# Performance work log

Hardware: AMD Instinct MI355X
Metric: run time of the kernel (lower is better)

The kernel has to match this reference:

```python
import jax, jax.numpy as jnp
import numpy as np

B, H, S, D = 2, 12, 4096, 768
BS = 64              # block size
HD = D // H          # head dim = 64
NB = S // BS         # 64 blocks
MC = 3               # max graph connections per block
PEN = -10000.0
RSQRT_D = 1.0 / np.sqrt(HD).astype(np.float32)


def setup_inputs() -> dict:
    key = jax.random.key(0)
    ks = jax.random.split(key, 6)
    hidden_states = jax.random.normal(ks[0], (B, S, D), jnp.float32)
    Wq = jax.random.normal(ks[1], (D, D), jnp.float32) * 0.02
    Wk = jax.random.normal(ks[2], (D, D), jnp.float32) * 0.02
    Wv = jax.random.normal(ks[3], (D, D), jnp.float32) * 0.02
    Wo = jax.random.normal(ks[4], (D, D), jnp.float32) * 0.02
    graph_attn = jax.random.randint(ks[5], (B, H, NB, MC), 0, NB, jnp.int32)
    return dict(
        hidden_states=hidden_states, Wq=Wq, Wk=Wk, Wv=Wv, Wo=Wo,
        band_mask=jnp.ones((B, 1, NB - 4, BS, 3 * BS), jnp.float32),
        from_mask=jnp.ones((B, 1, S, 1), jnp.float32),
        to_mask=jnp.ones((B, 1, 1, S), jnp.float32),
        from_blocked_mask=jnp.ones((B, NB, BS), jnp.float32),
        to_blocked_mask=jnp.ones((B, NB, BS), jnp.float32),
        graph_attn=graph_attn,
    )


def reference(hidden_states, Wq, Wk, Wv, Wo, band_mask, from_mask, to_mask,
              from_blocked_mask, to_blocked_mask, graph_attn):
    def proj(W):  # [B,S,D] -> [B,H,S,HD]
        return (hidden_states @ W.T).reshape(B, S, H, HD).transpose(0, 2, 1, 3)

    q, k, v = proj(Wq), proj(Wk), proj(Wv)
    bq = q.reshape(B, H, NB, BS, HD)
    bk = k.reshape(B, H, NB, BS, HD)
    bv = v.reshape(B, H, NB, BS, HD)

    # gather graph-selected key/value blocks: [B,H,NB,MC*BS,HD]
    gather = jax.vmap(jax.vmap(lambda blocks, idx: blocks[idx]))
    gk = gather(bk, graph_attn).reshape(B, H, NB, MC * BS, HD)
    gv = gather(bv, graph_attn).reshape(B, H, NB, MC * BS, HD)

    # graph mask from blocked masks: [B,H,NB,BS,MC*BS]
    gm = jax.vmap(lambda tm, ga: tm[ga])(to_blocked_mask, graph_attn)  # [B,H,NB,MC,BS]
    gm = gm.reshape(B, H, NB, MC * BS)
    graph_mask = jnp.einsum('blq,bhlk->bhlqk', from_blocked_mask, gm)

    # ---- first block: global attention over all keys ----
    fp = jnp.einsum('bhqd,bhkd->bhqk', bq[:, :, 0], k) * RSQRT_D + (1.0 - to_mask) * PEN
    first_ctx = jnp.einsum('bhqk,bhkd->bhqd', jax.nn.softmax(fp, -1), v)[:, :, None]

    # ---- second block: blocks 0,1,2,last + graph-gathered ----
    sk = jnp.concatenate([bk[:, :, 0], bk[:, :, 1], bk[:, :, 2], bk[:, :, -1], gk[:, :, 1]], axis=2)
    sv = jnp.concatenate([bv[:, :, 0], bv[:, :, 1], bv[:, :, 2], bv[:, :, -1], gv[:, :, 1]], axis=2)
    sp = jnp.einsum('bhqd,bhkd->bhqk', bq[:, :, 1], sk) * RSQRT_D
    seq_pad = jnp.concatenate([to_mask[:, :, :, :3 * BS], to_mask[:, :, :, -BS:],
                               jnp.ones((B, 1, 1, MC * BS), to_mask.dtype)], axis=3)
    rand_pad = jnp.concatenate([jnp.ones((B, H, BS, 4 * BS), graph_mask.dtype),
                                graph_mask[:, :, 1]], axis=3)
    sp = sp + (1.0 - jnp.minimum(seq_pad, rand_pad)) * PEN
    second_ctx = jnp.einsum('bhqk,bhkd->bhqd', jax.nn.softmax(sp, -1), sv)[:, :, None]

    # ---- middle blocks: sliding window (3 blocks) + first + last + graph ----
    ek = jnp.concatenate([bk[:, :, 1:-3], bk[:, :, 2:-2], bk[:, :, 3:-1]], axis=3)  # [B,H,NB-4,3BS,HD]
    ev = jnp.concatenate([bv[:, :, 1:-3], bv[:, :, 2:-2], bv[:, :, 3:-1]], axis=3)
    qm = bq[:, :, 2:-2]
    inner = jnp.einsum('bhlqd,bhlkd->bhlqk', qm, ek) * RSQRT_D + (1.0 - band_mask) * PEN
    randp = jnp.einsum('bhlqd,bhlkd->bhlqk', qm, gk[:, :, 2:-2]) * RSQRT_D + (1.0 - graph_mask[:, :, 2:-2]) * PEN
    firstp = jnp.einsum('bhlqd,bhkd->bhlqk', qm, bk[:, :, 0]) * RSQRT_D + (1.0 - to_mask[:, :, :, None, :BS]) * PEN
    lastp = jnp.einsum('bhlqd,bhkd->bhlqk', qm, bk[:, :, -1]) * RSQRT_D + (1.0 - to_mask[:, :, :, None, -BS:]) * PEN
    band = jnp.concatenate([firstp, inner, randp, lastp], axis=-1)
    attn = jax.nn.softmax(band, -1)
    mid_ctx = (jnp.einsum('bhlqk,bhlkd->bhlqd', attn[..., BS:4 * BS], ev)
               + jnp.einsum('bhlqk,bhlkd->bhlqd', attn[..., 4 * BS:4 * BS + MC * BS], gv[:, :, 2:-2])
               + jnp.einsum('bhlqk,bhkd->bhlqd', attn[..., :BS], bv[:, :, 0])
               + jnp.einsum('bhlqk,bhkd->bhlqd', attn[..., -BS:], bv[:, :, -1]))

    # ---- second-to-last block ----
    slk = jnp.concatenate([bk[:, :, 0], bk[:, :, -3], bk[:, :, -2], bk[:, :, -1], gk[:, :, -2]], axis=2)
    slv = jnp.concatenate([bv[:, :, 0], bv[:, :, -3], bv[:, :, -2], bv[:, :, -1], gv[:, :, -2]], axis=2)
    slp = jnp.einsum('bhqd,bhkd->bhqk', bq[:, :, -2], slk) * RSQRT_D
    sl_seq = jnp.concatenate([to_mask[:, :, :, :BS], to_mask[:, :, :, -3 * BS:],
                              jnp.ones((B, 1, 1, MC * BS), to_mask.dtype)], axis=3)
    sl_rand = jnp.concatenate([jnp.ones((B, H, BS, 4 * BS), graph_mask.dtype),
                               graph_mask[:, :, -2]], axis=3)
    slp = slp + (1.0 - jnp.minimum(sl_seq, sl_rand)) * PEN
    sl_ctx = jnp.einsum('bhqk,bhkd->bhqd', jax.nn.softmax(slp, -1), slv)[:, :, None]

    # ---- last block: global attention over all keys ----
    lp = jnp.einsum('bhqd,bhkd->bhqk', bq[:, :, -1], k) * RSQRT_D + (1.0 - to_mask) * PEN
    last_ctx = jnp.einsum('bhqk,bhkd->bhqd', jax.nn.softmax(lp, -1), v)[:, :, None]

    ctx = jnp.concatenate([first_ctx, second_ctx, mid_ctx, sl_ctx, last_ctx], axis=2)
    ctx = ctx.reshape(B, H, S, HD) * from_mask            # [B,H,S,HD]
    ctx = ctx.transpose(0, 2, 1, 3).reshape(B, S, D)      # [B,S,D]
    return ctx @ Wo.T                                     # output projection (no bias)
```

## Files before the change

kernel.cpp:

```cpp
#include <hip/hip_runtime.h>
#include <hip/hip_bf16.h>

#define BB 2
#define HH 12
#define SS 4096
#define DD 768
#define HD 64
#define NBK 64
#define MC 3

typedef __attribute__((ext_vector_type(8))) short short8_t;
typedef __attribute__((ext_vector_type(4))) float float4_t;

__device__ __forceinline__ unsigned short f2bf(float f) {
  union { float f; unsigned u; } c;
  c.f = f;
  unsigned u = c.u + 0x7FFFu + ((c.u >> 16) & 1u);
  return (unsigned short)(u >> 16);
}

__device__ __forceinline__ void gload16(const unsigned short* gp,
                                        unsigned short* lp) {
  __builtin_amdgcn_global_load_lds(
      (const __attribute__((address_space(1))) unsigned int*)gp,
      (__attribute__((address_space(3))) unsigned int*)lp, 16, 0, 0);
}

#define LDK 72

__global__ __launch_bounds__(256) void cvt_all(
    const float* __restrict__ hs, const float* __restrict__ Wq,
    const float* __restrict__ Wk, const float* __restrict__ Wv,
    const float* __restrict__ Wo, unsigned short* __restrict__ hsb,
    unsigned short* __restrict__ wqkvb, unsigned short* __restrict__ wob) {
  long i4 = (long)blockIdx.x * 256 + threadIdx.x;
  const float* src;
  unsigned short* dst;
  if (i4 < 1572864) {
    src = hs + i4 * 4;
    dst = hsb + i4 * 4;
  } else {
    long r = i4 - 1572864;
    int w = (int)(r / 147456);
    long e = r % 147456;
    src = (w == 0 ? Wq : w == 1 ? Wk : w == 2 ? Wv : Wo) + e * 4;
    dst = (w < 3) ? (wqkvb + (long)w * 589824 + e * 4) : (wob + e * 4);
  }
  float4_t v = *(const float4_t*)src;
  uint2 p;
  p.x = (unsigned)f2bf(v[0]) | ((unsigned)f2bf(v[1]) << 16);
  p.y = (unsigned)f2bf(v[2]) | ((unsigned)f2bf(v[3]) << 16);
  *(uint2*)dst = p;
}

#define STAGE_T(buf_, A_, B_, m0_, n0_, kt_)                                  \
  {                                                                           \
    int rr_ = lane >> 3;                                                      \
    int cg_ = (lane & 7) ^ rr_;                                               \
    _Pragma("unroll") for (int u = 0; u < 4; u++) {                           \
      int g_ = w * 4 + u;                                                     \
      gload16(A_ + (size_t)(m0_ + g_ * 8 + rr_) * DD + kt_ + cg_ * 8,         \
              &As[buf_][g_ * 512]);                                           \
    }                                                                         \
    _Pragma("unroll") for (int u = 0; u < 2; u++) {                           \
      int g_ = w * 2 + u;                                                     \
      gload16(B_ + (size_t)(n0_ + g_ * 8 + rr_) * DD + kt_ + cg_ * 8,         \
              &Bs[buf_][g_ * 512]);                                           \
    }                                                                         \
  }

#define LOAD_FRAGS2(buf_, kk_)                                                \
  int cb = qd + ((kk_) >> 3);                                                 \
  short8_t af[2], bfr[4];                                                     \
  _Pragma("unroll") for (int i = 0; i < 2; i++) {                             \
    int r_ = wm + i * 16 + fr;                                                \
    af[i] = *(const short8_t*)&As[buf_][r_ * 64 + (cb ^ (fr & 7)) * 8];       \
  }                                                                           \
  _Pragma("unroll") for (int j = 0; j < 4; j++) {                             \
    int r_ = j * 16 + fr;                                                     \
    bfr[j] = *(const short8_t*)&Bs[buf_][r_ * 64 + (cb ^ (fr & 7)) * 8];      \
  }

__global__ __launch_bounds__(256) void gemm_qkv_b(
    const unsigned short* __restrict__ A, const unsigned short* __restrict__ W,
    unsigned short* __restrict__ qb, unsigned short* __restrict__ kb,
    unsigned short* __restrict__ vtb) {
  __shared__ unsigned short As[2][128 * 64];
  __shared__ unsigned short Bs[2][64 * 64];
  int tid = threadIdx.x;
  int m0 = blockIdx.x * 128;
  int n0 = blockIdx.y * 64;
  int lane = tid & 63;
  int w = tid >> 6;
  int wm = w * 32;
  int fr = lane & 15;
  int qd = lane >> 4;
  int ysel = n0 / 768;

  float4_t acc[8];
#pragma unroll
  for (int i = 0; i < 8; i++)
#pragma unroll
    for (int r = 0; r < 4; r++) acc[i][r] = 0.f;

  STAGE_T(0, A, W, m0, n0, 0)
  int p = 0;

  if (ysel < 2) {
    for (int kt = 0; kt < DD; kt += 64) {
      __syncthreads();
      if (kt + 64 < DD) STAGE_T(p ^ 1, A, W, m0, n0, kt + 64)
#pragma unroll
      for (int kk = 0; kk < 64; kk += 32) {
        LOAD_FRAGS2(p, kk)
#pragma unroll
        for (int i = 0; i < 2; i++)
#pragma unroll
          for (int j = 0; j < 4; j++)
            acc[j * 2 + i] = __builtin_amdgcn_mfma_f32_16x16x32_bf16(
                bfr[j], af[i], acc[j * 2 + i], 0, 0, 0);
      }
      p ^= 1;
    }
    int cn = lane & 15;
    int quad = lane >> 4;
    float scale = (ysel == 0) ? 0.125f : 1.0f;
    unsigned short* dst = (ysel == 0) ? qb : kb;
    int nb0 = n0 - ysel * 768;
#pragma unroll
    for (int j = 0; j < 4; j++)
#pragma unroll
      for (int i = 0; i < 2; i++) {
        int m = m0 + wm + i * 16 + cn;
        int nn = nb0 + j * 16 + quad * 4;
        int b = m >> 12, s = m & 4095;
        int h = nn >> 6, d0 = nn & 63;
        uint2 pk;
        pk.x = (unsigned)f2bf(acc[j * 2 + i][0] * scale) |
               ((unsigned)f2bf(acc[j * 2 + i][1] * scale) << 16);
        pk.y = (unsigned)f2bf(acc[j * 2 + i][2] * scale) |
               ((unsigned)f2bf(acc[j * 2 + i][3] * scale) << 16);
        *(uint2*)&dst[(((size_t)b * HH + h) * SS + s) * HD + d0] = pk;
      }
  } else {
    for (int kt = 0; kt < DD; kt += 64) {
      __syncthreads();
      if (kt + 64 < DD) STAGE_T(p ^ 1, A, W, m0, n0, kt + 64)
#pragma unroll
      for (int kk = 0; kk < 64; kk += 32) {
        LOAD_FRAGS2(p, kk)
#pragma unroll
        for (int i = 0; i < 2; i++)
#pragma unroll
          for (int j = 0; j < 4; j++)
            acc[i * 4 + j] = __builtin_amdgcn_mfma_f32_16x16x32_bf16(
                af[i], bfr[j], acc[i * 4 + j], 0, 0, 0);
      }
      p ^= 1;
    }
    int cn = lane & 15;
    int quad = lane >> 4;
    int nb0 = n0 - 1536;
#pragma unroll
    for (int i = 0; i < 2; i++)
#pragma unroll
      for (int j = 0; j < 4; j++) {
        int m = m0 + wm + i * 16 + quad * 4;
        int nn = nb0 + j * 16 + cn;
        int b = m >> 12, s0 = m & 4095;
        int h = nn >> 6, d = nn & 63;
        uint2 pk;
        pk.x = (unsigned)f2bf(acc[i * 4 + j][0]) |
               ((unsigned)f2bf(acc[i * 4 + j][1]) << 16);
        pk.y = (unsigned)f2bf(acc[i * 4 + j][2]) |
               ((unsigned)f2bf(acc[i * 4 + j][3]) << 16);
        *(uint2*)&vtb[(((size_t)b * HH + h) * HD + d) * SS + s0] = pk;
      }
  }
}

__global__ __launch_bounds__(256) void gemm_out_b(
    const unsigned short* __restrict__ A, const unsigned short* __restrict__ W,
    float* __restrict__ dst) {
  __shared__ unsigned short As[2][128 * 64];
  __shared__ unsigned short Bs[2][64 * 64];
  int tid = threadIdx.x;
  int m0 = blockIdx.x * 128;
  int n0 = blockIdx.y * 64;
  int lane = tid & 63;
  int w = tid >> 6;
  int wm = w * 32;
  int fr = lane & 15;
  int qd = lane >> 4;

  float4_t acc[8];
#pragma unroll
  for (int i = 0; i < 8; i++)
#pragma unroll
    for (int r = 0; r < 4; r++) acc[i][r] = 0.f;

  STAGE_T(0, A, W, m0, n0, 0)
  int p = 0;
  for (int kt = 0; kt < DD; kt += 64) {
    __syncthreads();
    if (kt + 64 < DD) STAGE_T(p ^ 1, A, W, m0, n0, kt + 64)
#pragma unroll
    for (int kk = 0; kk < 64; kk += 32) {
      LOAD_FRAGS2(p, kk)
#pragma unroll
      for (int i = 0; i < 2; i++)
#pragma unroll
        for (int j = 0; j < 4; j++)
          acc[i * 4 + j] = __builtin_amdgcn_mfma_f32_16x16x32_bf16(
              af[i], bfr[j], acc[i * 4 + j], 0, 0, 0);
    }
    p ^= 1;
  }

  int cn = lane & 15;
  int rb = (lane >> 4) * 4;
#pragma unroll
  for (int i = 0; i < 2; i++)
#pragma unroll
    for (int j = 0; j < 4; j++)
#pragma unroll
      for (int r = 0; r < 4; r++) {
        int m = m0 + wm + i * 16 + rb + r;
        int n = n0 + j * 16 + cn;
        dst[(size_t)m * DD + n] = acc[i * 4 + j][r];
      }
}

__global__ __launch_bounds__(256) void attn2(
    const unsigned short* __restrict__ q, const unsigned short* __restrict__ k,
    const unsigned short* __restrict__ vt, const int* __restrict__ graph,
    unsigned short* __restrict__ ctxb, float* __restrict__ part) {
  __shared__ unsigned short Ks[2][64 * LDK];
  __shared__ unsigned short Vs[2][64 * LDK];
  __shared__ unsigned short Ps[4][16 * LDK];

  int tid = threadIdx.x;
  int id = blockIdx.x;
  int b, h, l, nkb, heavy, chunk = 0, hid = 0;
  int list[8];
  if (id < 384) {
    heavy = 1;
    hid = id >> 3;
    chunk = id & 7;
    b = hid / 24;
    int r = hid % 24;
    h = r >> 1;
    l = (r & 1) ? (NBK - 1) : 0;
    nkb = 8;
#pragma unroll
    for (int i = 0; i < 8; i++) list[i] = chunk * 8 + i;
  } else {
    heavy = 0;
    int j = id - 384;
    b = j / 744;
    int r = j % 744;
    h = r / 62;
    l = 1 + r % 62;
    const int* g = graph + (((size_t)b * HH + h) * NBK + l) * MC;
    int n = 0;
    if (l == 1) {
      list[0] = 0; list[1] = 1; list[2] = 2; list[3] = NBK - 1; n = 4;
    } else if (l == NBK - 2) {
      list[0] = 0; list[1] = NBK - 3; list[2] = NBK - 2; list[3] = NBK - 1; n = 4;
    } else {
      list[0] = 0; list[1] = l - 1; list[2] = l; list[3] = l + 1;
      list[4] = NBK - 1; n = 5;
    }
    for (int m = 0; m < MC; m++) list[n++] = g[m];
    nkb = n;
  }
  size_t base = ((size_t)b * HH + h) * SS * HD;

  int lane = tid & 63;
  int w = tid >> 6;
  int lr = lane & 15;
  int quad = lane >> 4;

  short8_t qa[2];
  {
    const unsigned short* qp =
        q + base + (size_t)(l * 64 + w * 16 + lr) * HD + quad * 8;
    qa[0] = *(const short8_t*)qp;
    qa[1] = *(const short8_t*)(qp + 32);
  }

  float4_t Ot[4];
  float ls[4];
#pragma unroll
  for (int t = 0; t < 4; t++)
#pragma unroll
    for (int r = 0; r < 4; r++) Ot[t][r] = 0.f;
#pragma unroll
  for (int r = 0; r < 4; r++) ls[r] = 0.f;

  int srow = tid >> 3;
  int scol = (tid & 7) * 8;

  uint4 kr0, kr1, vr0, vr1;
  {
    int kb = list[0];
    const unsigned short* kp = k + base + (size_t)(kb * 64 + srow) * HD + scol;
    const unsigned short* vp = vt + base + (size_t)srow * SS + kb * 64 + scol;
    kr0 = *(const uint4*)kp;
    kr1 = *(const uint4*)(kp + 32 * HD);
    vr0 = *(const uint4*)vp;
    vr1 = *(const uint4*)(vp + 32 * SS);
  }
  *(uint4*)&Ks[0][srow * LDK + scol] = kr0;
  *(uint4*)&Ks[0][(srow + 32) * LDK + scol] = kr1;
  *(uint4*)&Vs[0][srow * LDK + scol] = vr0;
  *(uint4*)&Vs[0][(srow + 32) * LDK + scol] = vr1;
  int p = 0;

  for (int t = 0; t < nkb; t++) {
    __syncthreads();

    if (t + 1 < nkb) {
      int kb = list[t + 1];
      const unsigned short* kp = k + base + (size_t)(kb * 64 + srow) * HD + scol;
      const unsigned short* vp = vt + base + (size_t)srow * SS + kb * 64 + scol;
      kr0 = *(const uint4*)kp;
      kr1 = *(const uint4*)(kp + 32 * HD);
      vr0 = *(const uint4*)vp;
      vr1 = *(const uint4*)(vp + 32 * SS);
    }

    float4_t st[4];
#pragma unroll
    for (int tt = 0; tt < 4; tt++) {
#pragma unroll
      for (int r = 0; r < 4; r++) st[tt][r] = 0.f;
      short8_t kb0 = *(const short8_t*)&Ks[p][(tt * 16 + lr) * LDK + quad * 8];
      short8_t kb1 =
          *(const short8_t*)&Ks[p][(tt * 16 + lr) * LDK + quad * 8 + 32];
      st[tt] = __builtin_amdgcn_mfma_f32_16x16x32_bf16(qa[0], kb0, st[tt], 0, 0, 0);
      st[tt] = __builtin_amdgcn_mfma_f32_16x16x32_bf16(qa[1], kb1, st[tt], 0, 0, 0);
    }

#pragma unroll
    for (int tt = 0; tt < 4; tt++)
#pragma unroll
      for (int r = 0; r < 4; r++) {
        float pv = __expf(st[tt][r]);
        st[tt][r] = pv;
        ls[r] += pv;
        Ps[w][(quad * 4 + r) * LDK + tt * 16 + lr] = f2bf(pv);
      }

#pragma unroll
    for (int s = 0; s < 2; s++) {
      short8_t pa = *(const short8_t*)&Ps[w][lr * LDK + s * 32 + quad * 8];
#pragma unroll
      for (int tt = 0; tt < 4; tt++) {
        short8_t vb =
            *(const short8_t*)&Vs[p][(tt * 16 + lr) * LDK + s * 32 + quad * 8];
        Ot[tt] = __builtin_amdgcn_mfma_f32_16x16x32_bf16(pa, vb, Ot[tt], 0, 0, 0);
      }
    }

    if (t + 1 < nkb) {
      *(uint4*)&Ks[p ^ 1][srow * LDK + scol] = kr0;
      *(uint4*)&Ks[p ^ 1][(srow + 32) * LDK + scol] = kr1;
      *(uint4*)&Vs[p ^ 1][srow * LDK + scol] = vr0;
      *(uint4*)&Vs[p ^ 1][(srow + 32) * LDK + scol] = vr1;
    }
    p ^= 1;
  }

#pragma unroll
  for (int r = 0; r < 4; r++)
#pragma unroll
    for (int off = 1; off < 16; off <<= 1) ls[r] += __shfl_xor(ls[r], off);

  if (!heavy) {
#pragma unroll
    for (int r = 0; r < 4; r++) {
      float inv = 1.f / ls[r];
      size_t row = (size_t)b * SS + (size_t)l * 64 + w * 16 + quad * 4 + r;
#pragma unroll
      for (int tt = 0; tt < 4; tt++)
        ctxb[row * DD + h * HD + tt * 16 + lr] = f2bf(Ot[tt][r] * inv);
    }
  } else {
    float* pb = part + ((size_t)hid * 8 + chunk) * 4160;
#pragma unroll
    for (int r = 0; r < 4; r++) {
      int rowi = w * 16 + quad * 4 + r;
#pragma unroll
      for (int tt = 0; tt < 4; tt++)
        pb[rowi * 64 + tt * 16 + lr] = Ot[tt][r];
      if (lr == 0) pb[4096 + rowi] = ls[r];
    }
  }
}

__global__ __launch_bounds__(256) void reduce_heavy(
    const float* __restrict__ part, unsigned short* __restrict__ ctxb) {
  __shared__ float lrow[64];
  int hid = blockIdx.x;
  int tid = threadIdx.x;
  int b = hid / 24;
  int r = hid % 24;
  int h = r >> 1;
  int l = (r & 1) ? (NBK - 1) : 0;
  const float* pb = part + (size_t)hid * 8 * 4160;
  if (tid < 64) {
    float s = 0.f;
#pragma unroll
    for (int c = 0; c < 8; c++) s += pb[c * 4160 + 4096 + tid];
    lrow[tid] = s;
  }
  __syncthreads();
#pragma unroll
  for (int e = tid; e < 4096; e += 256) {
    float o = 0.f;
#pragma unroll
    for (int c = 0; c < 8; c++) o += pb[c * 4160 + e];
    int rowi = e >> 6, col = e & 63;
    size_t row = (size_t)b * SS + (size_t)l * 64 + rowi;
    ctxb[row * DD + h * HD + col] = f2bf(o / lrow[rowi]);
  }
}

extern "C" void kernel_launch(void* const* d_in, const int* in_sizes, int n_in,
                              void* d_out, int out_size, void* d_ws,
                              size_t ws_size, hipStream_t stream) {
  const float* hs = (const float*)d_in[0];
  const float* Wq = (const float*)d_in[1];
  const float* Wk = (const float*)d_in[2];
  const float* Wv = (const float*)d_in[3];
  const float* Wo = (const float*)d_in[4];
  const int* graph = (const int*)d_in[10];

  const size_t NHS = (size_t)BB * SS * DD;
  unsigned short* hsb = (unsigned short*)d_ws;
  unsigned short* wqkvb = hsb + NHS;
  unsigned short* wob = wqkvb + 3 * 768 * 768;
  unsigned short* qb = wob + 768 * 768;
  unsigned short* kb = qb + NHS;
  unsigned short* vtb = kb + NHS;
  unsigned short* ctxb = vtb + NHS;
  float* part = (float*)(ctxb + NHS);

  cvt_all<<<8448, 256, 0, stream>>>(hs, Wq, Wk, Wv, Wo, hsb, wqkvb, wob);
  gemm_qkv_b<<<dim3(64, 36, 1), 256, 0, stream>>>(hsb, wqkvb, qb, kb, vtb);
  attn2<<<1872, 256, 0, stream>>>(qb, kb, vtb, graph, ctxb, part);
  reduce_heavy<<<48, 256, 0, stream>>>(part, ctxb);
  gemm_out_b<<<dim3(64, 12, 1), 256, 0, stream>>>(ctxb, wob, (float*)d_out);
}
```

Before: 209.5 us.

## Fuse fp32-to-bf16 conversion into GEMMs and fold heavy-row reduction into attention

Drops the separate conversion kernel. The QKV and output GEMMs now read fp32 inputs and weights directly, convert them to bf16 in registers with v_cvt_pk_bf16_f32, and store them into swizzled LDS. The separate reduce_heavy launch is replaced by an atomic-counter last-block reduction inside the attention kernel, and the QKV GEMM zeroes the counters. This saves a full read/write pass over the bf16 copies and two launches, at the cost of twice the global load bytes per GEMM tile, register-staged loads instead of direct-to-LDS loads, and the weights being reconverted by every tile.

```diff
diff --git a/kernel.cpp b/kernel.cpp
--- a/kernel.cpp
+++ b/kernel.cpp
@@ -8,6 +8,7 @@
 #define HD 64
 #define NBK 64
 #define MC 3
+#define LDK 72
 
 typedef __attribute__((ext_vector_type(8))) short short8_t;
 typedef __attribute__((ext_vector_type(4))) float float4_t;
@@ -19,6 +20,12 @@
   return (unsigned short)(u >> 16);
 }
 
+__device__ __forceinline__ unsigned cvtpk(float lo, float hi) {
+  unsigned r;
+  asm("v_cvt_pk_bf16_f32 %0, %1, %2" : "=v"(r) : "v"(lo), "v"(hi));
+  return r;
+}
+
 __device__ __forceinline__ void gload16(const unsigned short* gp,
                                         unsigned short* lp) {
   __builtin_amdgcn_global_load_lds(
@@ -26,107 +33,134 @@
       (__attribute__((address_space(3))) unsigned int*)lp, 16, 0, 0);
 }
 
-#define LDK 72
-
-__global__ __launch_bounds__(256) void cvt_all(
+__device__ __forceinline__ void cvt_store_A(unsigned short* buf, int arow,
+                                            int ah, const float4_t a4[8]) {
+#pragma unroll
+  for (int c2 = 0; c2 < 4; c2++) {
+    int chunk = 4 * ah + c2;
+    int slot = chunk ^ (arow & 7);
+    uint4 wv;
+    wv.x = cvtpk(a4[2 * c2][0], a4[2 * c2][1]);
+    wv.y = cvtpk(a4[2 * c2][2], a4[2 * c2][3]);
+    wv.z = cvtpk(a4[2 * c2 + 1][0], a4[2 * c2 + 1][1]);
+    wv.w = cvtpk(a4[2 * c2 + 1][2], a4[2 * c2 + 1][3]);
+    *(uint4*)&buf[arow * 64 + slot * 8] = wv;
+  }
+}
+
+__device__ __forceinline__ void cvt_store_B(unsigned short* buf, int brow,
+                                            int bq, const float4_t b4[4]) {
+#pragma unroll
+  for (int c2 = 0; c2 < 2; c2++) {
+    int chunk = 2 * bq + c2;
+    int slot = chunk ^ (brow & 7);
+    uint4 wv;
+    wv.x = cvtpk(b4[2 * c2][0], b4[2 * c2][1]);
+    wv.y = cvtpk(b4[2 * c2][2], b4[2 * c2][3]);
+    wv.z = cvtpk(b4[2 * c2 + 1][0], b4[2 * c2 + 1][1]);
+    wv.w = cvtpk(b4[2 * c2 + 1][2], b4[2 * c2 + 1][3]);
+    *(uint4*)&buf[brow * 64 + slot * 8] = wv;
+  }
+}
+
+template <int SWAP>
+__device__ __forceinline__ void gemm_cvt_core(const float* Ab, const float* Bb,
+                                              unsigned short* smem, int tid,
+                                              float4_t acc[8]) {
+  unsigned short* As = smem;
+  unsigned short* Bs = smem + 16384;
+  int lane = tid & 63, w = tid >> 6, wm = w * 32;
+  int fr = lane & 15, qd = lane >> 4;
+  int arow = tid >> 1, ah = tid & 1;
+  int brow = tid >> 2, bq = tid & 3;
+#pragma unroll
+  for (int i = 0; i < 8; i++)
+#pragma unroll
+    for (int r = 0; r < 4; r++) acc[i][r] = 0.f;
+
+  {
+    float4_t a4[8], b4[4];
+#pragma unroll
+    for (int u = 0; u < 8; u++) a4[u] = *(const float4_t*)(Ab + u * 4);
+#pragma unroll
+    for (int u = 0; u < 4; u++) b4[u] = *(const float4_t*)(Bb + u * 4);
+    cvt_store_A(As, arow, ah, a4);
+    cvt_store_B(Bs, brow, bq, b4);
+  }
+  int p = 0;
+  for (int kt = 0; kt < DD; kt += 64) {
+    __syncthreads();
+    bool more = (kt + 64 < DD);
+    float4_t a4[8], b4[4];
+    if (more) {
+#pragma unroll
+      for (int u = 0; u < 8; u++)
+        a4[u] = *(const float4_t*)(Ab + kt + 64 + u * 4);
+#pragma unroll
+      for (int u = 0; u < 4; u++)
+        b4[u] = *(const float4_t*)(Bb + kt + 64 + u * 4);
+    }
+#pragma unroll
+    for (int kk = 0; kk < 64; kk += 32) {
+      int cb = qd + (kk >> 3);
+      short8_t af[2], bfr[4];
+#pragma unroll
+      for (int i = 0; i < 2; i++) {
+        int r_ = wm + i * 16 + fr;
+        af[i] = *(const short8_t*)&As[p * 8192 + r_ * 64 + (cb ^ (fr & 7)) * 8];
+      }
+#pragma unroll
+      for (int j = 0; j < 4; j++) {
+        int r_ = j * 16 + fr;
+        bfr[j] =
+            *(const short8_t*)&Bs[p * 4096 + r_ * 64 + (cb ^ (fr & 7)) * 8];
+      }
+#pragma unroll
+      for (int i = 0; i < 2; i++)
+#pragma unroll
+        for (int j = 0; j < 4; j++) {
+          if (SWAP)
+            acc[j * 2 + i] = __builtin_amdgcn_mfma_f32_16x16x32_bf16(
+                bfr[j], af[i], acc[j * 2 + i], 0, 0, 0);
+          else
+            acc[i * 4 + j] = __builtin_amdgcn_mfma_f32_16x16x32_bf16(
+                af[i], bfr[j], acc[i * 4 + j], 0, 0, 0);
+        }
+    }
+    if (more) {
+      cvt_store_A(As + (p ^ 1) * 8192, arow, ah, a4);
+      cvt_store_B(Bs + (p ^ 1) * 4096, brow, bq, b4);
+    }
+    p ^= 1;
+  }
+}
+
+__global__ __launch_bounds__(256) void gemm_qkv_f(
     const float* __restrict__ hs, const float* __restrict__ Wq,
     const float* __restrict__ Wk, const float* __restrict__ Wv,
-    const float* __restrict__ Wo, unsigned short* __restrict__ hsb,
-    unsigned short* __restrict__ wqkvb, unsigned short* __restrict__ wob) {
-  long i4 = (long)blockIdx.x * 256 + threadIdx.x;
-  const float* src;
-  unsigned short* dst;
-  if (i4 < 1572864) {
-    src = hs + i4 * 4;
-    dst = hsb + i4 * 4;
-  } else {
-    long r = i4 - 1572864;
-    int w = (int)(r / 147456);
-    long e = r % 147456;
-    src = (w == 0 ? Wq : w == 1 ? Wk : w == 2 ? Wv : Wo) + e * 4;
-    dst = (w < 3) ? (wqkvb + (long)w * 589824 + e * 4) : (wob + e * 4);
-  }
-  float4_t v = *(const float4_t*)src;
-  uint2 p;
-  p.x = (unsigned)f2bf(v[0]) | ((unsigned)f2bf(v[1]) << 16);
-  p.y = (unsigned)f2bf(v[2]) | ((unsigned)f2bf(v[3]) << 16);
-  *(uint2*)dst = p;
-}
-
-#define STAGE_T(buf_, A_, B_, m0_, n0_, kt_)                                  \
-  {                                                                           \
-    int rr_ = lane >> 3;                                                      \
-    int cg_ = (lane & 7) ^ rr_;                                               \
-    _Pragma("unroll") for (int u = 0; u < 4; u++) {                           \
-      int g_ = w * 4 + u;                                                     \
-      gload16(A_ + (size_t)(m0_ + g_ * 8 + rr_) * DD + kt_ + cg_ * 8,         \
-              &As[buf_][g_ * 512]);                                           \
-    }                                                                         \
-    _Pragma("unroll") for (int u = 0; u < 2; u++) {                           \
-      int g_ = w * 2 + u;                                                     \
-      gload16(B_ + (size_t)(n0_ + g_ * 8 + rr_) * DD + kt_ + cg_ * 8,         \
-              &Bs[buf_][g_ * 512]);                                           \
-    }                                                                         \
-  }
-
-#define LOAD_FRAGS2(buf_, kk_)                                                \
-  int cb = qd + ((kk_) >> 3);                                                 \
-  short8_t af[2], bfr[4];                                                     \
-  _Pragma("unroll") for (int i = 0; i < 2; i++) {                             \
-    int r_ = wm + i * 16 + fr;                                                \
-    af[i] = *(const short8_t*)&As[buf_][r_ * 64 + (cb ^ (fr & 7)) * 8];       \
-  }                                                                           \
-  _Pragma("unroll") for (int j = 0; j < 4; j++) {                             \
-    int r_ = j * 16 + fr;                                                     \
-    bfr[j] = *(const short8_t*)&Bs[buf_][r_ * 64 + (cb ^ (fr & 7)) * 8];      \
-  }
-
-__global__ __launch_bounds__(256) void gemm_qkv_b(
-    const unsigned short* __restrict__ A, const unsigned short* __restrict__ W,
     unsigned short* __restrict__ qb, unsigned short* __restrict__ kb,
-    unsigned short* __restrict__ vtb) {
-  __shared__ unsigned short As[2][128 * 64];
-  __shared__ unsigned short Bs[2][64 * 64];
+    unsigned short* __restrict__ vtb, int* __restrict__ cnt) {
+  __shared__ __align__(16) unsigned short smem[24576];
   int tid = threadIdx.x;
+  if (blockIdx.x == 0 && blockIdx.y == 0 && tid < 48) cnt[tid] = 0;
   int m0 = blockIdx.x * 128;
   int n0 = blockIdx.y * 64;
-  int lane = tid & 63;
-  int w = tid >> 6;
-  int wm = w * 32;
-  int fr = lane & 15;
-  int qd = lane >> 4;
   int ysel = n0 / 768;
+  int nb0 = n0 - ysel * 768;
+  const float* Wsrc = (ysel == 0) ? Wq : (ysel == 1) ? Wk : Wv;
+  int lane = tid & 63, w = tid >> 6, wm = w * 32;
+  int arow = tid >> 1, ah = tid & 1;
+  int brow = tid >> 2, bq = tid & 3;
+  const float* Ab = hs + (size_t)(m0 + arow) * DD + ah * 32;
+  const float* Bb = Wsrc + (size_t)(nb0 + brow) * DD + bq * 16;
 
   float4_t acc[8];
-#pragma unroll
-  for (int i = 0; i < 8; i++)
-#pragma unroll
-    for (int r = 0; r < 4; r++) acc[i][r] = 0.f;
-
-  STAGE_T(0, A, W, m0, n0, 0)
-  int p = 0;
-
   if (ysel < 2) {
-    for (int kt = 0; kt < DD; kt += 64) {
-      __syncthreads();
-      if (kt + 64 < DD) STAGE_T(p ^ 1, A, W, m0, n0, kt + 64)
-#pragma unroll
-      for (int kk = 0; kk < 64; kk += 32) {
-        LOAD_FRAGS2(p, kk)
-#pragma unroll
-        for (int i = 0; i < 2; i++)
-#pragma unroll
-          for (int j = 0; j < 4; j++)
-            acc[j * 2 + i] = __builtin_amdgcn_mfma_f32_16x16x32_bf16(
-                bfr[j], af[i], acc[j * 2 + i], 0, 0, 0);
-      }
-      p ^= 1;
-    }
+    gemm_cvt_core<1>(Ab, Bb, smem, tid, acc);
     int cn = lane & 15;
     int quad = lane >> 4;
     float scale = (ysel == 0) ? 0.125f : 1.0f;
     unsigned short* dst = (ysel == 0) ? qb : kb;
-    int nb0 = n0 - ysel * 768;
 #pragma unroll
     for (int j = 0; j < 4; j++)
 #pragma unroll
@@ -143,24 +177,9 @@
         *(uint2*)&dst[(((size_t)b * HH + h) * SS + s) * HD + d0] = pk;
       }
   } else {
-    for (int kt = 0; kt < DD; kt += 64) {
-      __syncthreads();
-      if (kt + 64 < DD) STAGE_T(p ^ 1, A, W, m0, n0, kt + 64)
-#pragma unroll
-      for (int kk = 0; kk < 64; kk += 32) {
-        LOAD_FRAGS2(p, kk)
-#pragma unroll
-        for (int i = 0; i < 2; i++)
-#pragma unroll
-          for (int j = 0; j < 4; j++)
-            acc[i * 4 + j] = __builtin_amdgcn_mfma_f32_16x16x32_bf16(
-                af[i], bfr[j], acc[i * 4 + j], 0, 0, 0);
-      }
-      p ^= 1;
-    }
+    gemm_cvt_core<0>(Ab, Bb, smem, tid, acc);
     int cn = lane & 15;
     int quad = lane >> 4;
-    int nb0 = n0 - 1536;
 #pragma unroll
     for (int i = 0; i < 2; i++)
 #pragma unroll
@@ -179,19 +198,20 @@
   }
 }
 
-__global__ __launch_bounds__(256) void gemm_out_b(
-    const unsigned short* __restrict__ A, const unsigned short* __restrict__ W,
+__global__ __launch_bounds__(256) void gemm_out_f(
+    const unsigned short* __restrict__ A, const float* __restrict__ Wo,
     float* __restrict__ dst) {
-  __shared__ unsigned short As[2][128 * 64];
-  __shared__ unsigned short Bs[2][64 * 64];
+  __shared__ __align__(16) unsigned short smem[24576];
+  unsigned short* As = smem;
+  unsigned short* Bs = smem + 16384;
   int tid = threadIdx.x;
   int m0 = blockIdx.x * 128;
   int n0 = blockIdx.y * 64;
-  int lane = tid & 63;
-  int w = tid >> 6;
-  int wm = w * 32;
-  int fr = lane & 15;
-  int qd = lane >> 4;
+  int lane = tid & 63, w = tid >> 6, wm = w * 32;
+  int fr = lane & 15, qd = lane >> 4;
+  int brow = tid >> 2, bq = tid & 3;
+  int rr = lane >> 3, cgx = (lane & 7) ^ rr;
+  const float* Bb = Wo + (size_t)(n0 + brow) * DD + bq * 16;
 
   float4_t acc[8];
 #pragma unroll
@@ -199,14 +219,50 @@
 #pragma unroll
     for (int r = 0; r < 4; r++) acc[i][r] = 0.f;
 
-  STAGE_T(0, A, W, m0, n0, 0)
+  {
+#pragma unroll
+    for (int u = 0; u < 4; u++) {
+      int g = w * 4 + u;
+      gload16(A + (size_t)(m0 + g * 8 + rr) * DD + cgx * 8, &As[g * 512]);
+    }
+    float4_t b4[4];
+#pragma unroll
+    for (int u = 0; u < 4; u++) b4[u] = *(const float4_t*)(Bb + u * 4);
+    cvt_store_B(Bs, brow, bq, b4);
+  }
   int p = 0;
   for (int kt = 0; kt < DD; kt += 64) {
     __syncthreads();
-    if (kt + 64 < DD) STAGE_T(p ^ 1, A, W, m0, n0, kt + 64)
+    bool more = (kt + 64 < DD);
+    if (more) {
+#pragma unroll
+      for (int u = 0; u < 4; u++) {
+        int g = w * 4 + u;
+        gload16(A + (size_t)(m0 + g * 8 + rr) * DD + kt + 64 + cgx * 8,
+                &As[(p ^ 1) * 8192 + g * 512]);
+      }
+    }
+    float4_t b4[4];
+    if (more) {
+#pragma unroll
+      for (int u = 0; u < 4; u++)
+        b4[u] = *(const float4_t*)(Bb + kt + 64 + u * 4);
+    }
 #pragma unroll
     for (int kk = 0; kk < 64; kk += 32) {
-      LOAD_FRAGS2(p, kk)
+      int cb = qd + (kk >> 3);
+      short8_t af[2], bfr[4];
+#pragma unroll
+      for (int i = 0; i < 2; i++) {
+        int r_ = wm + i * 16 + fr;
+        af[i] = *(const short8_t*)&As[p * 8192 + r_ * 64 + (cb ^ (fr & 7)) * 8];
+      }
+#pragma unroll
+      for (int j = 0; j < 4; j++) {
+        int r_ = j * 16 + fr;
+        bfr[j] =
+            *(const short8_t*)&Bs[p * 4096 + r_ * 64 + (cb ^ (fr & 7)) * 8];
+      }
 #pragma unroll
       for (int i = 0; i < 2; i++)
 #pragma unroll
@@ -214,6 +270,7 @@
           acc[i * 4 + j] = __builtin_amdgcn_mfma_f32_16x16x32_bf16(
               af[i], bfr[j], acc[i * 4 + j], 0, 0, 0);
     }
+    if (more) cvt_store_B(Bs + (p ^ 1) * 4096, brow, bq, b4);
     p ^= 1;
   }
 
@@ -231,13 +288,15 @@
       }
 }
 
-__global__ __launch_bounds__(256) void attn2(
+__global__ __launch_bounds__(256) void attn2r(
     const unsigned short* __restrict__ q, const unsigned short* __restrict__ k,
     const unsigned short* __restrict__ vt, const int* __restrict__ graph,
-    unsigned short* __restrict__ ctxb, float* __restrict__ part) {
+    unsigned short* __restrict__ ctxb, float* __restrict__ part,
+    int* __restrict__ cnt) {
   __shared__ unsigned short Ks[2][64 * LDK];
   __shared__ unsigned short Vs[2][64 * LDK];
   __shared__ unsigned short Ps[4][16 * LDK];
+  __shared__ int isLast;
 
   int tid = threadIdx.x;
   int id = blockIdx.x;
@@ -266,7 +325,8 @@
     if (l == 1) {
       list[0] = 0; list[1] = 1; list[2] = 2; list[3] = NBK - 1; n = 4;
     } else if (l == NBK - 2) {
-      list[0] = 0; list[1] = NBK - 3; list[2] = NBK - 2; list[3] = NBK - 1; n = 4;
+      list[0] = 0; list[1] = NBK - 3; list[2] = NBK - 2; list[3] = NBK - 1;
+      n = 4;
     } else {
       list[0] = 0; list[1] = l - 1; list[2] = l; list[3] = l + 1;
       list[4] = NBK - 1; n = 5;
@@ -322,8 +382,10 @@
 
     if (t + 1 < nkb) {
       int kb = list[t + 1];
-      const unsigned short* kp = k + base + (size_t)(kb * 64 + srow) * HD + scol;
-      const unsigned short* vp = vt + base + (size_t)srow * SS + kb * 64 + scol;
+      const unsigned short* kp =
+          k + base + (size_t)(kb * 64 + srow) * HD + scol;
+      const unsigned short* vp =
+          vt + base + (size_t)srow * SS + kb * 64 + scol;
       kr0 = *(const uint4*)kp;
       kr1 = *(const uint4*)(kp + 32 * HD);
       vr0 = *(const uint4*)vp;
@@ -338,8 +400,10 @@
       short8_t kb0 = *(const short8_t*)&Ks[p][(tt * 16 + lr) * LDK + quad * 8];
       short8_t kb1 =
           *(const short8_t*)&Ks[p][(tt * 16 + lr) * LDK + quad * 8 + 32];
-      st[tt] = __builtin_amdgcn_mfma_f32_16x16x32_bf16(qa[0], kb0, st[tt], 0, 0, 0);
-      st[tt] = __builtin_amdgcn_mfma_f32_16x16x32_bf16(qa[1], kb1, st[tt], 0, 0, 0);
+      st[tt] =
+          __builtin_amdgcn_mfma_f32_16x16x32_bf16(qa[0], kb0, st[tt], 0, 0, 0);
+      st[tt] =
+          __builtin_amdgcn_mfma_f32_16x16x32_bf16(qa[1], kb1, st[tt], 0, 0, 0);
     }
 
 #pragma unroll
@@ -359,7 +423,8 @@
       for (int tt = 0; tt < 4; tt++) {
         short8_t vb =
             *(const short8_t*)&Vs[p][(tt * 16 + lr) * LDK + s * 32 + quad * 8];
-        Ot[tt] = __builtin_amdgcn_mfma_f32_16x16x32_bf16(pa, vb, Ot[tt], 0, 0, 0);
+        Ot[tt] =
+            __builtin_amdgcn_mfma_f32_16x16x32_bf16(pa, vb, Ot[tt], 0, 0, 0);
       }
     }
 
@@ -386,44 +451,40 @@
       for (int tt = 0; tt < 4; tt++)
         ctxb[row * DD + h * HD + tt * 16 + lr] = f2bf(Ot[tt][r] * inv);
     }
-  } else {
-    float* pb = part + ((size_t)hid * 8 + chunk) * 4160;
-#pragma unroll
-    for (int r = 0; r < 4; r++) {
-      int rowi = w * 16 + quad * 4 + r;
-#pragma unroll
-      for (int tt = 0; tt < 4; tt++)
-        pb[rowi * 64 + tt * 16 + lr] = Ot[tt][r];
-      if (lr == 0) pb[4096 + rowi] = ls[r];
-    }
-  }
-}
-
-__global__ __launch_bounds__(256) void reduce_heavy(
-    const float* __restrict__ part, unsigned short* __restrict__ ctxb) {
-  __shared__ float lrow[64];
-  int hid = blockIdx.x;
-  int tid = threadIdx.x;
-  int b = hid / 24;
-  int r = hid % 24;
-  int h = r >> 1;
-  int l = (r & 1) ? (NBK - 1) : 0;
-  const float* pb = part + (size_t)hid * 8 * 4160;
-  if (tid < 64) {
-    float s = 0.f;
-#pragma unroll
-    for (int c = 0; c < 8; c++) s += pb[c * 4160 + 4096 + tid];
-    lrow[tid] = s;
-  }
+    return;
+  }
+
+  float* pb = part + ((size_t)hid * 8 + chunk) * 4160;
+#pragma unroll
+  for (int r = 0; r < 4; r++) {
+    int rowi = w * 16 + quad * 4 + r;
+#pragma unroll
+    for (int tt = 0; tt < 4; tt++) pb[rowi * 64 + tt * 16 + lr] = Ot[tt][r];
+    if (lr == 0) pb[4096 + rowi] = ls[r];
+  }
+  __threadfence();
   __syncthreads();
-#pragma unroll
-  for (int e = tid; e < 4096; e += 256) {
-    float o = 0.f;
-#pragma unroll
-    for (int c = 0; c < 8; c++) o += pb[c * 4160 + e];
-    int rowi = e >> 6, col = e & 63;
-    size_t row = (size_t)b * SS + (size_t)l * 64 + rowi;
-    ctxb[row * DD + h * HD + col] = f2bf(o / lrow[rowi]);
+  if (tid == 0) isLast = (atomicAdd(&cnt[hid], 1) == 7);
+  __syncthreads();
+  if (isLast) {
+    __threadfence();
+    float* lrow = (float*)&Ks[0][0];
+    const float* pbase = part + (size_t)hid * 8 * 4160;
+    if (tid < 64) {
+      float s = 0.f;
+#pragma unroll
+      for (int c = 0; c < 8; c++) s += pbase[c * 4160 + 4096 + tid];
+      lrow[tid] = s;
+    }
+    __syncthreads();
+    for (int e = tid; e < 4096; e += 256) {
+      float o = 0.f;
+#pragma unroll
+      for (int c = 0; c < 8; c++) o += pbase[c * 4160 + e];
+      int rowi = e >> 6, col = e & 63;
+      size_t row = (size_t)b * SS + (size_t)l * 64 + rowi;
+      ctxb[row * DD + h * HD + col] = f2bf(o / lrow[rowi]);
+    }
   }
 }
 
@@ -438,18 +499,15 @@
   const int* graph = (const int*)d_in[10];
 
   const size_t NHS = (size_t)BB * SS * DD;
-  unsigned short* hsb = (unsigned short*)d_ws;
-  unsigned short* wqkvb = hsb + NHS;
-  unsigned short* wob = wqkvb + 3 * 768 * 768;
-  unsigned short* qb = wob + 768 * 768;
+  unsigned short* qb = (unsigned short*)d_ws;
   unsigned short* kb = qb + NHS;
   unsigned short* vtb = kb + NHS;
   unsigned short* ctxb = vtb + NHS;
   float* part = (float*)(ctxb + NHS);
-
-  cvt_all<<<8448, 256, 0, stream>>>(hs, Wq, Wk, Wv, Wo, hsb, wqkvb, wob);
-  gemm_qkv_b<<<dim3(64, 36, 1), 256, 0, stream>>>(hsb, wqkvb, qb, kb, vtb);
-  attn2<<<1872, 256, 0, stream>>>(qb, kb, vtb, graph, ctxb, part);
-  reduce_heavy<<<48, 256, 0, stream>>>(part, ctxb);
-  gemm_out_b<<<dim3(64, 12, 1), 256, 0, stream>>>(ctxb, wob, (float*)d_out);
-}
+  int* cnt = (int*)(part + 48 * 8 * 4160);
+
+  gemm_qkv_f<<<dim3(64, 36, 1), 256, 0, stream>>>(hs, Wq, Wk, Wv, qb, kb, vtb,
+                                                  cnt);
+  attn2r<<<1872, 256, 0, stream>>>(qb, kb, vtb, graph, ctxb, part, cnt);
+  gemm_out_f<<<dim3(64, 12, 1), 256, 0, stream>>>(ctxb, Wo, (float*)d_out);
+}
```

Result: slower. 367.0 us (+75.2%).
